# Kernel tuning notes

Hardware: AMD Instinct MI355X
Metric: run time of the kernel (lower is better)

The kernel has to match this reference:

```python
import jax, jax.numpy as jnp
import numpy as np
from jax import lax

RPN_BBOX_STD_DEV = np.array([0.1, 0.1, 0.2, 0.2], dtype=np.float32)
PRE_NMS_LIMIT = 6000
PROPOSAL_COUNT = 1000
NMS_THRESHOLD = 0.7


def apply_box_deltas(boxes, deltas):
    # boxes: [N,4] (y1,x1,y2,x2); deltas: [N,4] (dy,dx,log dh,log dw)
    h = boxes[:, 2] - boxes[:, 0]
    w = boxes[:, 3] - boxes[:, 1]
    cy = boxes[:, 0] + 0.5 * h + deltas[:, 0] * h
    cx = boxes[:, 1] + 0.5 * w + deltas[:, 1] * w
    h = h * jnp.exp(deltas[:, 2])
    w = w * jnp.exp(deltas[:, 3])
    y1 = cy - 0.5 * h
    x1 = cx - 0.5 * w
    return jnp.stack([y1, x1, y1 + h, x1 + w], axis=1)


def pairwise_iou(boxes):
    # boxes: [N,4] -> iou [N,N]
    y1, x1, y2, x2 = boxes[:, 0], boxes[:, 1], boxes[:, 2], boxes[:, 3]
    area = (y2 - y1) * (x2 - x1)
    iy1 = jnp.maximum(y1[:, None], y1[None, :])
    ix1 = jnp.maximum(x1[:, None], x1[None, :])
    iy2 = jnp.minimum(y2[:, None], y2[None, :])
    ix2 = jnp.minimum(x2[:, None], x2[None, :])
    inter = jnp.maximum(iy2 - iy1, 0.0) * jnp.maximum(ix2 - ix1, 0.0)
    union = area[:, None] + area[None, :] - inter
    return inter / jnp.maximum(union, 1e-12)


def nms_keep_mask(boxes, iou_threshold):
    # boxes are sorted by descending score; greedy suppression.
    n = boxes.shape[0]
    iou = pairwise_iou(boxes)  # [N,N]
    idxs = jnp.arange(n)

    def body(i, keep):
        suppressed = jnp.any((iou[i] > iou_threshold) & keep & (idxs < i))
        return keep.at[i].set(jnp.logical_not(suppressed))

    return lax.fori_loop(0, n, body, jnp.zeros((n,), dtype=bool))


def proposal_single(scores, deltas, anchors):
    # scores: [A], deltas: [A,4], anchors: [A,4] -- single image
    top_scores, ix = lax.top_k(scores, PRE_NMS_LIMIT)           # sorted desc
    d = deltas[ix] * RPN_BBOX_STD_DEV[None, :]
    boxes = apply_box_deltas(anchors[ix], d)
    boxes = jnp.clip(boxes, 0.0, 1.0)                           # window [0,0,1,1]
    keep = lax.stop_gradient(nms_keep_mask(boxes, NMS_THRESHOLD))
    # select top PROPOSAL_COUNT kept boxes in score order, pad with zeros
    masked = jnp.where(keep, top_scores, -jnp.inf)
    _, sel = lax.top_k(masked, PROPOSAL_COUNT)
    valid = keep[sel]
    props = jnp.where(valid[:, None], boxes[sel], 0.0)          # [P,4]
    return props


def reference(rpn_probs, rpn_bbox, anchors):
    scores = rpn_probs[:, :, 1]  # fg prob
    return jax.vmap(proposal_single)(scores, rpn_bbox, anchors)


def setup_inputs() -> dict:
    key = jax.random.key(0)
    k1, k2, k3, k4 = jax.random.split(key, 4)
    B, A = 8, 131072
    rpn_probs = jax.random.uniform(k1, (B, A, 2), dtype=jnp.float32)
    rpn_bbox = jax.random.normal(k2, (B, A, 4), dtype=jnp.float32)
    # valid normalized anchors: y1<y2, x1<x2, inside [0,1]
    tl = jax.random.uniform(k3, (B, A, 2), dtype=jnp.float32) * 0.9
    wh = jax.random.uniform(k4, (B, A, 2), dtype=jnp.float32) * 0.1 + 1e-3
    anchors = jnp.concatenate([tl, tl + wh], axis=-1)
    return {"rpn_probs": rpn_probs, "rpn_bbox": rpn_bbox, "anchors": anchors}
```

## Files before the change

kernel.cpp:

```cpp
#include <hip/hip_runtime.h>

#pragma clang fp contract(off)

typedef unsigned long long u64;
typedef unsigned int u32;
typedef unsigned short u16;

#define BATCH 8
#define NA 131072
#define NSEL 6000
#define NW 94
#define NPAD (NW * 64)
#define CAND_CAP 8192
#define PROP 1000
#define SCAP 2048
#define LDSE 12288
#define CELLCAP 256
#define LARGECAP 1024
#define LTHR 0.125f

#define OFF_HIST     0
#define OFF_BFILL    8256
#define OFF_SCNT     16512
#define OFF_CELLCNT  19584
#define MEMSET_BYTES 21696
#define OFF_DIAGT    21696
#define OFF_CAND     406720
#define OFF_BOXES    931008
#define OFF_CELLLIST 1701056
#define OFF_LARGE    1963200
#define OFF_SENT     1979584

__device__ __forceinline__ int bucket_of(u32 bits) {
  u32 hi = bits >> 16;
  if (hi >= 0x3E80u && hi < 0x3F80u) return (int)(hi - 0x3E80u);
  if (hi >= 0x3F80u && hi < 0x8000u) return 255;
  return -1;
}

__device__ __forceinline__ bool iou_gt(float4 A, float4 B, float areaA, float areaB) {
  float iy = fminf(A.z, B.z) - fmaxf(A.x, B.x);
  float ix = fminf(A.w, B.w) - fmaxf(A.y, B.y);
  float inter = fmaxf(iy, 0.0f) * fmaxf(ix, 0.0f);
  float uni = (areaA + areaB) - inter;
  float uc = fmaxf(uni, 1e-12f);
  return (double)inter >= 0x1.666667p-1 * (double)uc;
}

__device__ __forceinline__ void emit_pair(int b, int ra, int rb, u64* diagT,
                                          u32* sent, int* scnt) {
  int src = min(ra, rb), dst = max(ra, rb);
  int wsrc = src >> 6, wdst = dst >> 6;
  if (wsrc == wdst) {
    atomicOr(&diagT[((size_t)b * NW + wdst) * 64 + (dst & 63)], 1ULL << (src & 63));
  } else {
    int e = atomicAdd(&scnt[b * NW + wdst], 1);
    if (e < SCAP)
      sent[(size_t)(b * NW + wdst) * SCAP + e] = ((u32)src << 6) | (u32)(dst & 63);
  }
}

__device__ __forceinline__ u64 shfl_xor_u64(u64 v, int lanemask) {
  u32 lo = (u32)v, hi = (u32)(v >> 32);
  lo = (u32)__shfl_xor((int)lo, lanemask);
  hi = (u32)__shfl_xor((int)hi, lanemask);
  return ((u64)hi << 32) | (u64)lo;
}

__device__ __forceinline__ void prefix_from_hist(const int* __restrict__ hist, int b,
                                                 int* h, int* bst, int* tb_s) {
  if (threadIdx.x < 256) h[threadIdx.x] = hist[b * 257 + threadIdx.x];
  __syncthreads();
  if (threadIdx.x == 0) {
    int run = 0, t = 0;
    bool found = false;
    for (int v = 255; v >= 0; --v) {
      bst[v] = run;
      run += h[v];
      if (!found && run >= NSEL) { t = v; found = true; }
    }
    *tb_s = t;
  }
  __syncthreads();
}

__global__ __launch_bounds__(256) void hist_kernel(const float* __restrict__ probs,
                                                   int* __restrict__ hist) {
  int b = blockIdx.y;
  const float2* p2 = reinterpret_cast<const float2*>(probs);
  __shared__ int h[257];
  for (int i = threadIdx.x; i < 257; i += 256) h[i] = 0;
  __syncthreads();
  int stride = gridDim.x * blockDim.x;
  for (int a = blockIdx.x * blockDim.x + threadIdx.x; a < NA; a += stride) {
    float sc = p2[(size_t)b * NA + a].y;
    int bk = bucket_of(__float_as_uint(sc));
    atomicAdd(&h[bk < 0 ? 256 : bk], 1);
  }
  __syncthreads();
  for (int i = threadIdx.x; i < 257; i += 256)
    if (h[i]) atomicAdd(&hist[b * 257 + i], h[i]);
}

__global__ __launch_bounds__(256) void gather_kernel(const float* __restrict__ probs,
                                                     const int* __restrict__ hist,
                                                     int* __restrict__ bfill,
                                                     u64* __restrict__ cand) {
  int b = blockIdx.y;
  const float2* p2 = reinterpret_cast<const float2*>(probs);
  __shared__ int h[256];
  __shared__ int bst[256];
  __shared__ int tb_s;
  prefix_from_hist(hist, b, h, bst, &tb_s);
  int tb = tb_s;
  int stride = gridDim.x * blockDim.x;
  for (int a = blockIdx.x * blockDim.x + threadIdx.x; a < NA; a += stride) {
    float sc = p2[(size_t)b * NA + a].y;
    u32 bits = __float_as_uint(sc);
    int bk = bucket_of(bits);
    if (bk >= tb) {
      int pos = bst[bk] + atomicAdd(&bfill[b * 257 + bk], 1);
      if (pos < CAND_CAP)
        cand[(size_t)b * CAND_CAP + pos] = ((u64)bits << 32) | (u64)(0xFFFFFFFFu - (u32)a);
    }
  }
}

__global__ __launch_bounds__(256) void sortdecode_kernel(const int* __restrict__ hist,
                                                         const int* __restrict__ bfill,
                                                         const u64* __restrict__ cand,
                                                         const float* __restrict__ anchors,
                                                         const float* __restrict__ deltas,
                                                         float4* __restrict__ boxes,
                                                         int* __restrict__ cellCnt,
                                                         u16* __restrict__ cellList,
                                                         u16* __restrict__ largeList,
                                                         u64* __restrict__ diagT) {
  int b = blockIdx.y;
  int tid = threadIdx.x;
  {
    int g = blockIdx.x * 256 + tid;
    if (g < NW * 64) diagT[(size_t)b * NW * 64 + g] = 0ULL;
  }
  __shared__ int h[256];
  __shared__ int bst[256];
  __shared__ int tb_s;
  prefix_from_hist(hist, b, h, bst, &tb_s);
  if (blockIdx.x == 0) {
    float4 z = {0.f, 0.f, 0.f, 0.f};
    for (int r = NSEL + tid; r < NPAD; r += 256) boxes[(size_t)b * NPAD + r] = z;
  }
  int v = tb_s + blockIdx.x;
  if (v > 255) return;
  int start = bst[v];
  if (start >= NSEL) return;
  int cnt = min(min(bfill[b * 257 + v], 1024), CAND_CAP - start);
  if (cnt <= 0) return;
  const u64* seg = cand + (size_t)b * CAND_CAP + start;
  __shared__ u64 s[1024];
  u64 x[4];
#pragma unroll
  for (int p = 0; p < 4; ++p) {
    int i = p * 256 + tid;
    x[p] = (i < cnt) ? seg[i] : 0ULL;
  }
  for (int k = 2; k <= 64; k <<= 1) {
    for (int j = k >> 1; j >= 1; j >>= 1) {
#pragma unroll
      for (int p = 0; p < 4; ++p) {
        int i = p * 256 + tid;
        u64 pv = shfl_xor_u64(x[p], j);
        bool takemax = (((i & j) == 0) == ((i & k) == 0));
        u64 mx = x[p] > pv ? x[p] : pv;
        u64 mn = x[p] < pv ? x[p] : pv;
        x[p] = takemax ? mx : mn;
      }
    }
  }
#pragma unroll
  for (int p = 0; p < 4; ++p) s[p * 256 + tid] = x[p];
  __syncthreads();
  for (int k = 128; k <= 1024; k <<= 1) {
    for (int j = k >> 1; j >= 64; j >>= 1) {
      for (int q = tid; q < 512; q += 256) {
        int i = ((q & ~(j - 1)) << 1) | (q & (j - 1));
        int ixj = i | j;
        u64 a = s[i], c = s[ixj];
        bool up = ((i & k) == 0);
        if (up ? (a < c) : (a > c)) { s[i] = c; s[ixj] = a; }
      }
      __syncthreads();
    }
#pragma unroll
    for (int p = 0; p < 4; ++p) x[p] = s[p * 256 + tid];
    for (int j = 32; j >= 1; j >>= 1) {
#pragma unroll
      for (int p = 0; p < 4; ++p) {
        int i = p * 256 + tid;
        u64 pv = shfl_xor_u64(x[p], j);
        bool takemax = (((i & j) == 0) == ((i & k) == 0));
        u64 mx = x[p] > pv ? x[p] : pv;
        u64 mn = x[p] < pv ? x[p] : pv;
        x[p] = takemax ? mx : mn;
      }
    }
    __syncthreads();
#pragma unroll
    for (int p = 0; p < 4; ++p) s[p * 256 + tid] = x[p];
    __syncthreads();
  }
  for (int i = tid; i < cnt; i += 256) {
    int r = start + i;
    if (r >= NSEL) continue;
    u64 key = s[i];
    float4 o = {0.f, 0.f, 0.f, 0.f};
    u32 idx = 0xFFFFFFFFu - (u32)(key & 0xFFFFFFFFu);
    if (idx < NA) {
      float4 av = *reinterpret_cast<const float4*>(anchors + ((size_t)b * NA + idx) * 4);
      float4 dv = *reinterpret_cast<const float4*>(deltas + ((size_t)b * NA + idx) * 4);
      float y1 = av.x, x1 = av.y, y2 = av.z, x2 = av.w;
      float dy = dv.x * 0.1f, dx = dv.y * 0.1f;
      float dh = dv.z * 0.2f, dw = dv.w * 0.2f;
      float hh = y2 - y1, ww = x2 - x1;
      float cy = y1 + 0.5f * hh + dy * hh;
      float cx = x1 + 0.5f * ww + dx * ww;
      hh = hh * expf(dh);
      ww = ww * expf(dw);
      float ny1 = cy - 0.5f * hh, nx1 = cx - 0.5f * ww;
      float ny2 = ny1 + hh, nx2 = nx1 + ww;
      o.x = fminf(fmaxf(ny1, 0.f), 1.f);
      o.y = fminf(fmaxf(nx1, 0.f), 1.f);
      o.z = fminf(fmaxf(ny2, 0.f), 1.f);
      o.w = fminf(fmaxf(nx2, 0.f), 1.f);
    }
    boxes[(size_t)b * NPAD + r] = o;
    float bh = o.z - o.x, bw = o.w - o.y;
    if (bh > LTHR || bw > LTHR) {
      int pos = atomicAdd(&cellCnt[b * 65 + 64], 1);
      if (pos < LARGECAP) largeList[b * LARGECAP + pos] = (u16)r;
    } else {
      int gy = min(7, max(0, (int)((o.x + o.z) * 4.0f)));
      int gx = min(7, max(0, (int)((o.y + o.w) * 4.0f)));
      int cell = gy * 8 + gx;
      int pos = atomicAdd(&cellCnt[b * 65 + cell], 1);
      if (pos < CELLCAP) cellList[((size_t)b * 64 + cell) * CELLCAP + pos] = (u16)r;
    }
  }
}

__global__ __launch_bounds__(256) void pairs_kernel(const float4* __restrict__ boxes,
                                                    const u16* __restrict__ cellList,
                                                    const u16* __restrict__ largeList,
                                                    const int* __restrict__ cellCnt,
                                                    u64* __restrict__ diagT,
                                                    u32* __restrict__ sent,
                                                    int* __restrict__ scnt) {
  int b = blockIdx.y;
  int tid = threadIdx.x;
  if (blockIdx.x >= 64) {
    int lb = blockIdx.x - 64;
    int nL = min(cellCnt[b * 65 + 64], LARGECAP);
    if (nL == 0) return;
    for (int li = lb; li < nL; li += 64) {
      int L = largeList[b * LARGECAP + li];
      float4 Lb = boxes[(size_t)b * NPAD + L];
      float hL = Lb.z - Lb.x, wL = Lb.w - Lb.y;
      if (0.7f * hL >= 0.126f || 0.7f * wL >= 0.126f) continue;
      float La = hL * wL;
      float sLy = Lb.x + Lb.z, sLx = Lb.y + Lb.w;
      int gy0 = max(0, (int)((sLy - 0.08f) * 4.0f));
      int gy1 = min(7, (int)((sLy + 0.08f) * 4.0f));
      int gx0 = max(0, (int)((sLx - 0.08f) * 4.0f));
      int gx1 = min(7, (int)((sLx + 0.08f) * 4.0f));
      for (int gy = gy0; gy <= gy1; ++gy)
        for (int gx = gx0; gx <= gx1; ++gx) {
          int cc = gy * 8 + gx;
          int cnt = min(cellCnt[b * 65 + cc], CELLCAP);
          for (int i = tid; i < cnt; i += 256) {
            int r = cellList[((size_t)b * 64 + cc) * CELLCAP + i];
            float4 jb = boxes[(size_t)b * NPAD + r];
            float ja = (jb.z - jb.x) * (jb.w - jb.y);
            if (iou_gt(Lb, jb, La, ja)) emit_pair(b, L, r, diagT, sent, scnt);
          }
        }
    }
    int s = 1;
    while ((1 << s) < nL) ++s;
    int tot = nL << s, m = (1 << s) - 1;
    int stride = 64 * 256;
    for (int t = lb * 256 + tid; t < tot; t += stride) {
      int i = t >> s, j = t & m;
      if (j >= nL || i >= j) continue;
      int Li = largeList[b * LARGECAP + i];
      int Lj = largeList[b * LARGECAP + j];
      float4 A = boxes[(size_t)b * NPAD + Li];
      float4 B = boxes[(size_t)b * NPAD + Lj];
      float aA = (A.z - A.x) * (A.w - A.y);
      float aB = (B.z - B.x) * (B.w - B.y);
      if (iou_gt(A, B, aA, aB)) emit_pair(b, Li, Lj, diagT, sent, scnt);
    }
    return;
  }
  int c = blockIdx.x;
  int cy = c >> 3, cx = c & 7;
  int nA = min(cellCnt[b * 65 + c], CELLCAP);
  if (nA == 0) return;
  __shared__ float4 Ab[CELLCAP];
  __shared__ float Aa[CELLCAP];
  __shared__ float Asx[CELLCAP];
  __shared__ float Asy[CELLCAP];
  __shared__ u16 Ai[CELLCAP];
  __shared__ u16 fAi[CELLCAP];
  __shared__ float4 Bb[3 * CELLCAP];
  __shared__ float Ba[3 * CELLCAP];
  __shared__ u16 Bi[3 * CELLCAP];
  __shared__ int nfA_s, nfB_s;
  for (int i = tid; i < nA; i += 256) {
    int r = cellList[((size_t)b * 64 + c) * CELLCAP + i];
    float4 bx = boxes[(size_t)b * NPAD + r];
    Ab[i] = bx;
    Aa[i] = (bx.z - bx.x) * (bx.w - bx.y);
    Asy[i] = bx.x + bx.z;
    Asx[i] = bx.y + bx.w;
    Ai[i] = (u16)r;
  }
  __syncthreads();
  {
    int totS = (nA * (nA - 1)) >> 1;
    for (int t = tid; t < totS; t += 256) {
      int i = (int)((1.0f + sqrtf(8.0f * (float)t + 1.0f)) * 0.5f);
      int tri = (i * (i - 1)) >> 1;
      if (t < tri) {
        --i;
        tri = (i * (i - 1)) >> 1;
      } else if (t >= tri + i) {
        tri += i;
        ++i;
      }
      int j = t - tri;
      if (iou_gt(Ab[i], Ab[j], Aa[i], Aa[j]))
        emit_pair(b, Ai[i], Ai[j], diagT, sent, scnt);
    }
  }
  if (cx < 7) {
    __syncthreads();
    if (tid == 0) { nfA_s = 0; nfB_s = 0; }
    __syncthreads();
    float XR2 = (float)(cx + 1) * 0.25f;
    for (int i = tid; i < nA; i += 256)
      if (Asx[i] > XR2 - 0.078f) fAi[atomicAdd(&nfA_s, 1)] = (u16)i;
    int nc = c + 1;
    int nN = min(cellCnt[b * 65 + nc], CELLCAP);
    for (int i = tid; i < nN; i += 256) {
      int r = cellList[((size_t)b * 64 + nc) * CELLCAP + i];
      float4 bx = boxes[(size_t)b * NPAD + r];
      if (bx.y + bx.w < XR2 + 0.078f) {
        int p = atomicAdd(&nfB_s, 1);
        Bb[p] = bx;
        Ba[p] = (bx.z - bx.x) * (bx.w - bx.y);
        Bi[p] = (u16)r;
      }
    }
    __syncthreads();
    int nfA = nfA_s, nfB = nfB_s;
    if (nfA && nfB) {
      int s = 1;
      while ((1 << s) < nfB) ++s;
      int tot = nfA << s, m = (1 << s) - 1;
      for (int t = tid; t < tot; t += 256) {
        int ii = fAi[t >> s], j = t & m;
        if (j < nfB && iou_gt(Ab[ii], Bb[j], Aa[ii], Ba[j]))
          emit_pair(b, Ai[ii], Bi[j], diagT, sent, scnt);
      }
    }
  }
  if (cy < 7) {
    __syncthreads();
    if (tid == 0) { nfA_s = 0; nfB_s = 0; }
    __syncthreads();
    float YB2 = (float)(cy + 1) * 0.25f;
    float XL2 = (float)cx * 0.25f;
    float XR2 = (float)(cx + 1) * 0.25f;
    for (int i = tid; i < nA; i += 256)
      if (Asy[i] > YB2 - 0.078f) fAi[atomicAdd(&nfA_s, 1)] = (u16)i;
    for (int k = 0; k < 3; ++k) {
      int nx = cx + k - 1;
      if (nx < 0 || nx > 7) continue;
      int nc = (cy + 1) * 8 + nx;
      int nN = min(cellCnt[b * 65 + nc], CELLCAP);
      for (int i = tid; i < nN; i += 256) {
        int r = cellList[((size_t)b * 64 + nc) * CELLCAP + i];
        float4 bx = boxes[(size_t)b * NPAD + r];
        float bsy = bx.x + bx.z, bsx = bx.y + bx.w;
        bool ok = bsy < YB2 + 0.078f;
        if (k == 0) ok = ok && (bsx > XL2 - 0.078f);
        if (k == 2) ok = ok && (bsx < XR2 + 0.078f);
        if (ok) {
          int p = atomicAdd(&nfB_s, 1);
          Bb[p] = bx;
          Ba[p] = (bx.z - bx.x) * (bx.w - bx.y);
          Bi[p] = (u16)r;
        }
      }
    }
    __syncthreads();
    int nfA = nfA_s, nfB = nfB_s;
    if (nfA && nfB) {
      int s = 1;
      while ((1 << s) < nfB) ++s;
      int tot = nfA << s, m = (1 << s) - 1;
      for (int t = tid; t < tot; t += 256) {
        int ii = fAi[t >> s], j = t & m;
        if (j < nfB && iou_gt(Ab[ii], Bb[j], Aa[ii], Ba[j]))
          emit_pair(b, Ai[ii], Bi[j], diagT, sent, scnt);
      }
    }
  }
}

__global__ __launch_bounds__(1024) void nms_kernel(const u32* __restrict__ sent,
                                                   const int* __restrict__ scnt,
                                                   const u64* __restrict__ diagT,
                                                   const float4* __restrict__ boxes,
                                                   float4* __restrict__ out) {
  int b = blockIdx.x;
  int tid = threadIdx.x;
  int lane = tid & 63;
  int wv = tid >> 6;
  __shared__ u64 diag_s[NW * 64];
  __shared__ u32 entS[LDSE];
  __shared__ u32 rmb[NW * 64];
  __shared__ int cw[NW];
  __shared__ int prefix[NW + 1];
  __shared__ u64 Kw_s[NW];
  __shared__ int baseW[NW];
  for (int i = tid; i < NW * 64; i += 1024) {
    diag_s[i] = diagT[(size_t)b * NW * 64 + i];
    rmb[i] = 0u;
  }
  if (tid < NW) cw[tid] = min(scnt[b * NW + tid], SCAP);
  {
    float4 z = {0.f, 0.f, 0.f, 0.f};
    for (int i = tid; i < PROP; i += 1024) out[(size_t)b * PROP + i] = z;
  }
  __syncthreads();
  if (tid == 0) {
    int run = 0;
    for (int w = 0; w < NW; ++w) { prefix[w] = run; run += cw[w]; }
    prefix[NW] = run;
  }
  __syncthreads();
  for (int w = wv; w < NW; w += 16) {
    const u32* gb = sent + (size_t)(b * NW + w) * SCAP;
    int base = prefix[w], n = cw[w];
    for (int e = lane; e < n; e += 64) {
      int slot = base + e;
      if (slot < LDSE) entS[slot] = gb[e];
    }
  }
  __syncthreads();
  if (wv == 0) {
    int total = 0;
    u64 cmask = diag_s[lane];
    u32 entp = 0;
    {
      int n0 = cw[0];
      if (lane < n0) {
        int slot = prefix[0] + lane;
        entp = (slot < LDSE) ? entS[slot] : sent[(size_t)(b * NW) * SCAP + lane];
      }
    }
    for (int w = 0; w < NW; ++w) {
      u64 cmask_next = (w + 1 < NW) ? diag_s[(w + 1) * 64 + lane] : 0ULL;
      int n = cw[w], base = prefix[w];
      u32 entn = 0;
      int nn = (w + 1 < NW) ? cw[w + 1] : 0;
      if (lane < nn) {
        int slot = prefix[w + 1] + lane;
        entn = (slot < LDSE) ? entS[slot]
                             : sent[(size_t)(b * NW + w + 1) * SCAP + lane];
      }
      if (lane < n) {
        int srcr = (int)(entp >> 6);
        if ((Kw_s[srcr >> 6] >> (srcr & 63)) & 1ULL) rmb[w * 64 + (entp & 63)] = 1u;
      }
      for (int e = lane + 64; e < n; e += 64) {
        int slot = base + e;
        u32 ent = (slot < LDSE) ? entS[slot] : sent[(size_t)(b * NW + w) * SCAP + e];
        int srcr = (int)(ent >> 6);
        if ((Kw_s[srcr >> 6] >> (srcr & 63)) & 1ULL) rmb[w * 64 + (ent & 63)] = 1u;
      }
      u32 rb = rmb[w * 64 + lane];
      u64 validm = (w * 64 + 64 <= NSEL) ? ~0ULL : ((1ULL << (NSEL - w * 64)) - 1ULL);
      bool alive0 = (rb == 0u) && ((validm >> lane) & 1ULL);
      u64 K = __ballot(alive0);
      for (int it = 0; it < 70; ++it) {
        bool alive = alive0 && ((K & cmask) == 0ULL);
        u64 Kn = __ballot(alive);
        if (Kn == K) break;
        K = Kn;
      }
      if (lane == 0) {
        Kw_s[w] = K;
        baseW[w] = total;
      }
      total += __popcll(K);
      cmask = cmask_next;
      entp = entn;
    }
  }
  __syncthreads();
  for (int i = tid; i < NSEL; i += 1024) {
    int w = i >> 6, bb = i & 63;
    u64 K = Kw_s[w];
    if ((K >> bb) & 1ULL) {
      int rank = baseW[w] + __popcll(K & ((1ULL << bb) - 1ULL));
      if (rank < PROP) out[(size_t)b * PROP + rank] = boxes[(size_t)b * NPAD + i];
    }
  }
}

extern "C" void kernel_launch(void* const* d_in, const int* in_sizes, int n_in,
                              void* d_out, int out_size, void* d_ws, size_t ws_size,
                              hipStream_t stream) {
  const float* probs = (const float*)d_in[0];
  const float* deltas = (const float*)d_in[1];
  const float* anchors = (const float*)d_in[2];
  char* ws = (char*)d_ws;
  int* hist = (int*)(ws + OFF_HIST);
  int* bfill = (int*)(ws + OFF_BFILL);
  int* scnt = (int*)(ws + OFF_SCNT);
  int* cellCnt = (int*)(ws + OFF_CELLCNT);
  u64* diagT = (u64*)(ws + OFF_DIAGT);
  u64* cand = (u64*)(ws + OFF_CAND);
  float4* boxes = (float4*)(ws + OFF_BOXES);
  u16* cellList = (u16*)(ws + OFF_CELLLIST);
  u16* largeList = (u16*)(ws + OFF_LARGE);
  u32* sent = (u32*)(ws + OFF_SENT);

  (void)hipMemsetAsync(ws, 0, MEMSET_BYTES, stream);

  hist_kernel<<<dim3(64, BATCH), 256, 0, stream>>>(probs, hist);
  gather_kernel<<<dim3(64, BATCH), 256, 0, stream>>>(probs, hist, bfill, cand);
  sortdecode_kernel<<<dim3(64, BATCH), 256, 0, stream>>>(hist, bfill, cand, anchors,
                                                         deltas, boxes, cellCnt,
                                                         cellList, largeList, diagT);
  pairs_kernel<<<dim3(128, BATCH), 256, 0, stream>>>(boxes, cellList, largeList,
                                                     cellCnt, diagT, sent, scnt);
  nms_kernel<<<BATCH, 1024, 0, stream>>>(sent, scnt, diagT, boxes, (float4*)d_out);
}
```

Before: 234.6 us.

## Group NMS into 256-box tiles with dense intra-tile masks held in registers

Replaces the 64-box word blocks of the serial NMS scan with 256-box tiles. Suppression pairs inside a tile are stored as a dense 4-word bitmask per box, and the scanning wave prefetches the next tile's masks into registers. Only cross-tile pairs go through the sparse edge lists. This cuts the number of serial outer iterations, and with them the LDS edge-list passes and barriers on the critical single-wave path. In exchange it adds register pressure, a larger workspace to clear, and a four-step sequential sub-word resolve inside each tile.

```diff
diff --git a/kernel.cpp b/kernel.cpp
--- a/kernel.cpp
+++ b/kernel.cpp
@@ -9,11 +9,13 @@
 #define BATCH 8
 #define NA 131072
 #define NSEL 6000
-#define NW 94
-#define NPAD (NW * 64)
+#define NT 24
+#define TILE 256
+#define NWORD (NT * 4)
+#define NPAD (NT * TILE)
 #define CAND_CAP 8192
 #define PROP 1000
-#define SCAP 2048
+#define SCAP 4096
 #define LDSE 12288
 #define CELLCAP 256
 #define LARGECAP 1024
@@ -22,14 +24,14 @@
 #define OFF_HIST     0
 #define OFF_BFILL    8256
 #define OFF_SCNT     16512
-#define OFF_CELLCNT  19584
-#define MEMSET_BYTES 21696
-#define OFF_DIAGT    21696
-#define OFF_CAND     406720
-#define OFF_BOXES    931008
-#define OFF_CELLLIST 1701056
-#define OFF_LARGE    1963200
-#define OFF_SENT     1979584
+#define OFF_CELLCNT  17344
+#define MEMSET_BYTES 19456
+#define OFF_TILET    19456
+#define OFF_CAND     1592320
+#define OFF_BOXES    2116608
+#define OFF_CELLLIST 2903040
+#define OFF_LARGE    3165184
+#define OFF_SENT     3181568
 
 __device__ __forceinline__ int bucket_of(u32 bits) {
   u32 hi = bits >> 16;
@@ -47,16 +49,17 @@
   return (double)inter >= 0x1.666667p-1 * (double)uc;
 }
 
-__device__ __forceinline__ void emit_pair(int b, int ra, int rb, u64* diagT,
+__device__ __forceinline__ void emit_pair(int b, int ra, int rb, u64* tileT,
                                           u32* sent, int* scnt) {
   int src = min(ra, rb), dst = max(ra, rb);
-  int wsrc = src >> 6, wdst = dst >> 6;
-  if (wsrc == wdst) {
-    atomicOr(&diagT[((size_t)b * NW + wdst) * 64 + (dst & 63)], 1ULL << (src & 63));
+  int tsrc = src >> 8, tdst = dst >> 8;
+  if (tsrc == tdst) {
+    atomicOr(&tileT[(((size_t)b * NT + tdst) * TILE + (dst & 255)) * 4 + ((src >> 6) & 3)],
+             1ULL << (src & 63));
   } else {
-    int e = atomicAdd(&scnt[b * NW + wdst], 1);
+    int e = atomicAdd(&scnt[b * NT + tdst], 1);
     if (e < SCAP)
-      sent[(size_t)(b * NW + wdst) * SCAP + e] = ((u32)src << 6) | (u32)(dst & 63);
+      sent[(size_t)(b * NT + tdst) * SCAP + e] = ((u32)src << 8) | (u32)(dst & 255);
   }
 }
 
@@ -65,6 +68,13 @@
   lo = (u32)__shfl_xor((int)lo, lanemask);
   hi = (u32)__shfl_xor((int)hi, lanemask);
   return ((u64)hi << 32) | (u64)lo;
+}
+
+__device__ __forceinline__ u64 valid_mask(int g) {
+  int lo = g * 64;
+  if (lo + 64 <= NSEL) return ~0ULL;
+  if (lo >= NSEL) return 0ULL;
+  return (1ULL << (NSEL - lo)) - 1ULL;
 }
 
 __device__ __forceinline__ void prefix_from_hist(const int* __restrict__ hist, int b,
@@ -135,13 +145,11 @@
                                                          int* __restrict__ cellCnt,
                                                          u16* __restrict__ cellList,
                                                          u16* __restrict__ largeList,
-                                                         u64* __restrict__ diagT) {
+                                                         u64* __restrict__ tileT) {
   int b = blockIdx.y;
   int tid = threadIdx.x;
-  {
-    int g = blockIdx.x * 256 + tid;
-    if (g < NW * 64) diagT[(size_t)b * NW * 64 + g] = 0ULL;
-  }
+  for (int g = blockIdx.x * 256 + tid; g < NT * TILE * 4; g += 64 * 256)
+    tileT[(size_t)b * (NT * TILE * 4) + g] = 0ULL;
   __shared__ int h[256];
   __shared__ int bst[256];
   __shared__ int tb_s;
@@ -252,7 +260,7 @@
                                                     const u16* __restrict__ cellList,
                                                     const u16* __restrict__ largeList,
                                                     const int* __restrict__ cellCnt,
-                                                    u64* __restrict__ diagT,
+                                                    u64* __restrict__ tileT,
                                                     u32* __restrict__ sent,
                                                     int* __restrict__ scnt) {
   int b = blockIdx.y;
@@ -280,7 +288,7 @@
             int r = cellList[((size_t)b * 64 + cc) * CELLCAP + i];
             float4 jb = boxes[(size_t)b * NPAD + r];
             float ja = (jb.z - jb.x) * (jb.w - jb.y);
-            if (iou_gt(Lb, jb, La, ja)) emit_pair(b, L, r, diagT, sent, scnt);
+            if (iou_gt(Lb, jb, La, ja)) emit_pair(b, L, r, tileT, sent, scnt);
           }
         }
     }
@@ -297,7 +305,7 @@
       float4 B = boxes[(size_t)b * NPAD + Lj];
       float aA = (A.z - A.x) * (A.w - A.y);
       float aB = (B.z - B.x) * (B.w - B.y);
-      if (iou_gt(A, B, aA, aB)) emit_pair(b, Li, Lj, diagT, sent, scnt);
+      if (iou_gt(A, B, aA, aB)) emit_pair(b, Li, Lj, tileT, sent, scnt);
     }
     return;
   }
@@ -339,7 +347,7 @@
       }
       int j = t - tri;
       if (iou_gt(Ab[i], Ab[j], Aa[i], Aa[j]))
-        emit_pair(b, Ai[i], Ai[j], diagT, sent, scnt);
+        emit_pair(b, Ai[i], Ai[j], tileT, sent, scnt);
     }
   }
   if (cx < 7) {
@@ -370,7 +378,7 @@
       for (int t = tid; t < tot; t += 256) {
         int ii = fAi[t >> s], j = t & m;
         if (j < nfB && iou_gt(Ab[ii], Bb[j], Aa[ii], Ba[j]))
-          emit_pair(b, Ai[ii], Bi[j], diagT, sent, scnt);
+          emit_pair(b, Ai[ii], Bi[j], tileT, sent, scnt);
       }
     }
   }
@@ -412,47 +420,44 @@
       for (int t = tid; t < tot; t += 256) {
         int ii = fAi[t >> s], j = t & m;
         if (j < nfB && iou_gt(Ab[ii], Bb[j], Aa[ii], Ba[j]))
-          emit_pair(b, Ai[ii], Bi[j], diagT, sent, scnt);
-      }
-    }
-  }
-}
-
-__global__ __launch_bounds__(1024) void nms_kernel(const u32* __restrict__ sent,
-                                                   const int* __restrict__ scnt,
-                                                   const u64* __restrict__ diagT,
-                                                   const float4* __restrict__ boxes,
-                                                   float4* __restrict__ out) {
+          emit_pair(b, Ai[ii], Bi[j], tileT, sent, scnt);
+      }
+    }
+  }
+}
+
+__global__ __launch_bounds__(512) void nms_kernel(const u32* __restrict__ sent,
+                                                  const int* __restrict__ scnt,
+                                                  const u64* __restrict__ tileT,
+                                                  const float4* __restrict__ boxes,
+                                                  float4* __restrict__ out) {
   int b = blockIdx.x;
   int tid = threadIdx.x;
   int lane = tid & 63;
   int wv = tid >> 6;
-  __shared__ u64 diag_s[NW * 64];
   __shared__ u32 entS[LDSE];
-  __shared__ u32 rmb[NW * 64];
-  __shared__ int cw[NW];
-  __shared__ int prefix[NW + 1];
-  __shared__ u64 Kw_s[NW];
-  __shared__ int baseW[NW];
-  for (int i = tid; i < NW * 64; i += 1024) {
-    diag_s[i] = diagT[(size_t)b * NW * 64 + i];
-    rmb[i] = 0u;
-  }
-  if (tid < NW) cw[tid] = min(scnt[b * NW + tid], SCAP);
+  __shared__ u32 rmb[TILE];
+  __shared__ u64 Kall[NWORD];
+  __shared__ int cw[NT];
+  __shared__ int prefix[NT + 1];
+  __shared__ int baseT[NT];
+  if (tid < NT) cw[tid] = min(scnt[b * NT + tid], SCAP);
+  if (tid < TILE) rmb[tid] = 0u;
+  if (tid < NWORD) Kall[tid] = 0ULL;
   {
     float4 z = {0.f, 0.f, 0.f, 0.f};
-    for (int i = tid; i < PROP; i += 1024) out[(size_t)b * PROP + i] = z;
+    for (int i = tid; i < PROP; i += 512) out[(size_t)b * PROP + i] = z;
   }
   __syncthreads();
   if (tid == 0) {
     int run = 0;
-    for (int w = 0; w < NW; ++w) { prefix[w] = run; run += cw[w]; }
-    prefix[NW] = run;
-  }
-  __syncthreads();
-  for (int w = wv; w < NW; w += 16) {
-    const u32* gb = sent + (size_t)(b * NW + w) * SCAP;
-    int base = prefix[w], n = cw[w];
+    for (int t = 0; t < NT; ++t) { prefix[t] = run; run += cw[t]; }
+    prefix[NT] = run;
+  }
+  __syncthreads();
+  for (int t = wv; t < NT; t += 8) {
+    const u32* gb = sent + (size_t)(b * NT + t) * SCAP;
+    int base = prefix[t], n = cw[t];
     for (int e = lane; e < n; e += 64) {
       int slot = base + e;
       if (slot < LDSE) entS[slot] = gb[e];
@@ -460,61 +465,114 @@
   }
   __syncthreads();
   if (wv == 0) {
+    const u64* tb0 = tileT + (size_t)b * (NT * TILE * 4);
+    u64 mc[4][4], mn[4][4];
+#pragma unroll
+    for (int q = 0; q < 4; ++q)
+#pragma unroll
+      for (int j = 0; j < 4; ++j)
+        mc[q][j] = tb0[(size_t)(q * 64 + lane) * 4 + j];
     int total = 0;
-    u64 cmask = diag_s[lane];
-    u32 entp = 0;
-    {
-      int n0 = cw[0];
-      if (lane < n0) {
-        int slot = prefix[0] + lane;
-        entp = (slot < LDSE) ? entS[slot] : sent[(size_t)(b * NW) * SCAP + lane];
-      }
-    }
-    for (int w = 0; w < NW; ++w) {
-      u64 cmask_next = (w + 1 < NW) ? diag_s[(w + 1) * 64 + lane] : 0ULL;
-      int n = cw[w], base = prefix[w];
-      u32 entn = 0;
-      int nn = (w + 1 < NW) ? cw[w + 1] : 0;
-      if (lane < nn) {
-        int slot = prefix[w + 1] + lane;
-        entn = (slot < LDSE) ? entS[slot]
-                             : sent[(size_t)(b * NW + w + 1) * SCAP + lane];
-      }
-      if (lane < n) {
-        int srcr = (int)(entp >> 6);
-        if ((Kw_s[srcr >> 6] >> (srcr & 63)) & 1ULL) rmb[w * 64 + (entp & 63)] = 1u;
-      }
-      for (int e = lane + 64; e < n; e += 64) {
-        int slot = base + e;
-        u32 ent = (slot < LDSE) ? entS[slot] : sent[(size_t)(b * NW + w) * SCAP + e];
-        int srcr = (int)(ent >> 6);
-        if ((Kw_s[srcr >> 6] >> (srcr & 63)) & 1ULL) rmb[w * 64 + (ent & 63)] = 1u;
-      }
-      u32 rb = rmb[w * 64 + lane];
-      u64 validm = (w * 64 + 64 <= NSEL) ? ~0ULL : ((1ULL << (NSEL - w * 64)) - 1ULL);
-      bool alive0 = (rb == 0u) && ((validm >> lane) & 1ULL);
-      u64 K = __ballot(alive0);
-      for (int it = 0; it < 70; ++it) {
-        bool alive = alive0 && ((K & cmask) == 0ULL);
-        u64 Kn = __ballot(alive);
-        if (Kn == K) break;
-        K = Kn;
+    for (int t = 0; t < NT; ++t) {
+      if (t + 1 < NT) {
+        const u64* nb = tb0 + (size_t)(t + 1) * (TILE * 4);
+#pragma unroll
+        for (int q = 0; q < 4; ++q)
+#pragma unroll
+          for (int j = 0; j < 4; ++j)
+            mn[q][j] = nb[(size_t)(q * 64 + lane) * 4 + j];
+      }
+      {
+        int n = cw[t], base = prefix[t];
+        for (int e = lane; e < n; e += 64) {
+          int slot = base + e;
+          u32 ent = (slot < LDSE) ? entS[slot] : sent[(size_t)(b * NT + t) * SCAP + e];
+          int srcr = (int)(ent >> 8);
+          if ((Kall[srcr >> 6] >> (srcr & 63)) & 1ULL) rmb[ent & 255] = 1u;
+        }
+      }
+      u32 f0 = rmb[lane], f1 = rmb[64 + lane], f2 = rmb[128 + lane], f3 = rmb[192 + lane];
+      rmb[lane] = 0u;
+      rmb[64 + lane] = 0u;
+      rmb[128 + lane] = 0u;
+      rmb[192 + lane] = 0u;
+      int gw = t * 4;
+      u64 K0, K1, K2, K3;
+      {
+        bool alive0 = (f0 == 0u) && ((valid_mask(gw) >> lane) & 1ULL);
+        u64 cm = mc[0][0];
+        u64 K = __ballot(alive0);
+        for (int it = 0; it < 70; ++it) {
+          bool alive = alive0 && ((K & cm) == 0ULL);
+          u64 Kn = __ballot(alive);
+          if (Kn == K) break;
+          K = Kn;
+        }
+        K0 = K;
+      }
+      {
+        u64 pre = K0 & mc[1][0];
+        bool alive0 = (f1 == 0u) && ((valid_mask(gw + 1) >> lane) & 1ULL) && (pre == 0ULL);
+        u64 cm = mc[1][1];
+        u64 K = __ballot(alive0);
+        for (int it = 0; it < 70; ++it) {
+          bool alive = alive0 && ((K & cm) == 0ULL);
+          u64 Kn = __ballot(alive);
+          if (Kn == K) break;
+          K = Kn;
+        }
+        K1 = K;
+      }
+      {
+        u64 pre = (K0 & mc[2][0]) | (K1 & mc[2][1]);
+        bool alive0 = (f2 == 0u) && ((valid_mask(gw + 2) >> lane) & 1ULL) && (pre == 0ULL);
+        u64 cm = mc[2][2];
+        u64 K = __ballot(alive0);
+        for (int it = 0; it < 70; ++it) {
+          bool alive = alive0 && ((K & cm) == 0ULL);
+          u64 Kn = __ballot(alive);
+          if (Kn == K) break;
+          K = Kn;
+        }
+        K2 = K;
+      }
+      {
+        u64 pre = (K0 & mc[3][0]) | (K1 & mc[3][1]) | (K2 & mc[3][2]);
+        bool alive0 = (f3 == 0u) && ((valid_mask(gw + 3) >> lane) & 1ULL) && (pre == 0ULL);
+        u64 cm = mc[3][3];
+        u64 K = __ballot(alive0);
+        for (int it = 0; it < 70; ++it) {
+          bool alive = alive0 && ((K & cm) == 0ULL);
+          u64 Kn = __ballot(alive);
+          if (Kn == K) break;
+          K = Kn;
+        }
+        K3 = K;
       }
       if (lane == 0) {
-        Kw_s[w] = K;
-        baseW[w] = total;
-      }
-      total += __popcll(K);
-      cmask = cmask_next;
-      entp = entn;
-    }
-  }
-  __syncthreads();
-  for (int i = tid; i < NSEL; i += 1024) {
-    int w = i >> 6, bb = i & 63;
-    u64 K = Kw_s[w];
+        Kall[gw] = K0;
+        Kall[gw + 1] = K1;
+        Kall[gw + 2] = K2;
+        Kall[gw + 3] = K3;
+        baseT[t] = total;
+      }
+      total += __popcll(K0) + __popcll(K1) + __popcll(K2) + __popcll(K3);
+#pragma unroll
+      for (int q = 0; q < 4; ++q)
+#pragma unroll
+        for (int j = 0; j < 4; ++j)
+          mc[q][j] = mn[q][j];
+    }
+  }
+  __syncthreads();
+  for (int i = tid; i < NSEL; i += 512) {
+    int g = i >> 6, bb = i & 63;
+    u64 K = Kall[g];
     if ((K >> bb) & 1ULL) {
-      int rank = baseW[w] + __popcll(K & ((1ULL << bb) - 1ULL));
+      int t = i >> 8;
+      int rank = baseT[t];
+      for (int q = t * 4; q < g; ++q) rank += __popcll(Kall[q]);
+      rank += __popcll(K & ((1ULL << bb) - 1ULL));
       if (rank < PROP) out[(size_t)b * PROP + rank] = boxes[(size_t)b * NPAD + i];
     }
   }
@@ -531,7 +589,7 @@
   int* bfill = (int*)(ws + OFF_BFILL);
   int* scnt = (int*)(ws + OFF_SCNT);
   int* cellCnt = (int*)(ws + OFF_CELLCNT);
-  u64* diagT = (u64*)(ws + OFF_DIAGT);
+  u64* tileT = (u64*)(ws + OFF_TILET);
   u64* cand = (u64*)(ws + OFF_CAND);
   float4* boxes = (float4*)(ws + OFF_BOXES);
   u16* cellList = (u16*)(ws + OFF_CELLLIST);
@@ -544,8 +602,8 @@
   gather_kernel<<<dim3(64, BATCH), 256, 0, stream>>>(probs, hist, bfill, cand);
   sortdecode_kernel<<<dim3(64, BATCH), 256, 0, stream>>>(hist, bfill, cand, anchors,
                                                          deltas, boxes, cellCnt,
-                                                         cellList, largeList, diagT);
+                                                         cellList, largeList, tileT);
   pairs_kernel<<<dim3(128, BATCH), 256, 0, stream>>>(boxes, cellList, largeList,
-                                                     cellCnt, diagT, sent, scnt);
-  nms_kernel<<<BATCH, 1024, 0, stream>>>(sent, scnt, diagT, boxes, (float4*)d_out);
-}
+                                                     cellCnt, tileT, sent, scnt);
+  nms_kernel<<<BATCH, 512, 0, stream>>>(sent, scnt, tileT, boxes, (float4*)d_out);
+}
```

New measurement: 218.8 us. 6.7% less time.
